# Kernel optimization log

Hardware: AMD Instinct MI355X
Metric: run time of the kernel (lower is better)

## Reference

```python
import math
import jax, jax.numpy as jnp
import numpy as np

BATCH = 2048
LATENT = 64
BETA = 6.0
LOG_2PI = math.log(2.0 * math.pi)


def setup_inputs() -> dict:
    key = jax.random.key(0)
    k1, k2, k3 = jax.random.split(key, 3)
    z = jax.random.normal(k1, (BATCH, LATENT), dtype=jnp.float32)
    z_mean = jax.random.normal(k2, (BATCH, LATENT), dtype=jnp.float32)
    z_logvar = jax.random.normal(k3, (BATCH, LATENT), dtype=jnp.float32)
    return {"z": z, "z_mean": z_mean, "z_logvar": z_logvar}


def _gaussian_log_density(samples, mean, log_var):
    # elementwise Gaussian log-density, broadcasts to [B, B, L]
    inv_sigma = jnp.exp(-log_var)
    tmp = samples - mean
    return -0.5 * (tmp * tmp * inv_sigma + log_var + LOG_2PI)


def _total_correlation(z, z_mean, z_logvar):
    # log q(z_i | x_j) per-dim: [B, B, L]
    log_qz_prob = _gaussian_log_density(z[:, None, :], z_mean[None, :, :], z_logvar[None, :, :])
    # log prod_l (1/B) sum_j q(z_l | x_j)  (constants dropped as in original)
    log_qz_product = jnp.sum(jax.scipy.special.logsumexp(log_qz_prob, axis=1), axis=1)  # [B]
    # log (1/B) sum_j q(z | x_j)
    log_qz = jax.scipy.special.logsumexp(jnp.sum(log_qz_prob, axis=2), axis=1)  # [B]
    return jnp.mean(log_qz - log_qz_product)


def _gaussian_kl(z_mean, z_logvar):
    # standard KL(q(z|x) || N(0, I)), mean over batch
    return 0.5 * jnp.mean(
        jnp.sum(jnp.square(z_mean) + jnp.exp(z_logvar) - z_logvar - 1.0, axis=1)
    )


def reference(z, z_mean, z_logvar):
    kl_loss = _gaussian_kl(z_mean, z_logvar)
    tc = (BETA - 1.0) * _total_correlation(z, z_mean, z_logvar)
    return tc + kl_loss
```

## Files before the change

### kernel.cpp

```cpp
#include <hip/hip_runtime.h>
#include <hip/hip_bf16.h>
#include <math.h>

#define BATCH 2048
#define LATENT 64
#define LOG_2PI 1.8378770664093453f
#define BETA_M1 5.0f
#define LN2 0.69314718055994530942f
#define C2 (-0.72134752044448170368f)

#define OFF_VT   0
#define OFF_TCE  (128*BATCH)
#define OFF_UP   (OFF_TCE + 64*BATCH)
#define OFF_CE   (OFF_UP + 128*BATCH)
#define OFF_KLP  (OFF_CE + BATCH)
#define OFF_RMP  (OFF_KLP + BATCH)
#define OFF_RSP  (OFF_RMP + 2*BATCH)
#define OFF_PART (OFF_RSP + 2*BATCH)
#define OFF_PP   (OFF_PART + 16)

__global__ __launch_bounds__(256) void precompute_kernel(const float* __restrict__ z,
                                                         const float* __restrict__ zm,
                                                         const float* __restrict__ zlv,
                                                         float* __restrict__ ws) {
    __shared__ float Tz[16][65], Tm[16][65], Tlv[16][65];
    __shared__ float CEp[16][16], KLp[16][16];
    int t = threadIdx.x, lane = t & 63, w = t >> 6;
    int j0 = blockIdx.x * 16;

    #pragma unroll
    for (int p = 0; p < 4; ++p) {
        int jr = p * 4 + w;
        int idx = (j0 + jr) * LATENT + lane;
        Tz[jr][lane]  = z[idx];
        Tm[jr][lane]  = zm[idx];
        Tlv[jr][lane] = zlv[idx];
    }
    if (blockIdx.x == 0 && t < 16) ws[OFF_PART + t] = 0.0f;
    __syncthreads();

    int jl = t & 15, lg = t >> 4;
    int j = j0 + jl;
    float ce_acc = 0.0f, kl_acc = 0.0f;
    #pragma unroll
    for (int q = 0; q < 4; ++q) {
        int l = q * 16 + lg;
        float zv = Tz[jl][l];
        float m  = Tm[jl][l];
        float lv = Tlv[jl][l];
        float iv  = __expf(-lv);
        float civ = C2 * iv;
        float miv = m * iv;
        float cmv = C2 * miv;
        float cev = C2 * fmaf(m, miv, lv + LOG_2PI);
        ws[OFF_VT  + (2*l)   * BATCH + j] = civ;
        ws[OFF_VT  + (2*l+1) * BATCH + j] = cmv;
        ws[OFF_TCE + l       * BATCH + j] = cev;
        ws[OFF_UP  + (2*l)   * BATCH + j] = zv * zv;
        ws[OFF_UP  + (2*l+1) * BATCH + j] = -2.0f * zv;
        ce_acc += cev;
        kl_acc += fmaf(m, m, __expf(lv)) - lv - 1.0f;
    }
    CEp[lg][jl] = ce_acc;
    KLp[lg][jl] = kl_acc;
    __syncthreads();
    if (t < 16) {
        float ce = 0.0f, kl = 0.0f;
        #pragma unroll
        for (int g = 0; g < 16; ++g) { ce += CEp[g][t]; kl += KLp[g][t]; }
        ws[OFF_CE  + j0 + t] = ce;
        ws[OFF_KLP + j0 + t] = kl;
    }
}

#define DIMB 512
#define ROWB 512
__global__ __launch_bounds__(256) void main_kernel(float* __restrict__ ws) {
    __shared__ float RMs[8][4], RSs[8][4];
    int bx = blockIdx.x, t = threadIdx.x;

    if (bx < DIMB) {
        int l  = bx >> 3;
        int jc = bx & 7;

        const float* __restrict__ up0 = ws + OFF_UP + (2*l)   * BATCH;
        const float* __restrict__ up1 = ws + OFF_UP + (2*l+1) * BATCH;
        float z2[8], n2[8];
        #pragma unroll
        for (int k = 0; k < 8; ++k) {
            z2[k] = up0[t + 256*k];
            n2[k] = up1[t + 256*k];
        }

        const float* __restrict__ pc = ws + OFF_VT  + (2*l)   * BATCH + jc * 256;
        const float* __restrict__ pm = ws + OFF_VT  + (2*l+1) * BATCH + jc * 256;
        const float* __restrict__ pe = ws + OFF_TCE + l       * BATCH + jc * 256;

        float s[8];
        #pragma unroll
        for (int k = 0; k < 8; ++k) s[k] = 0.0f;

        for (int jj = 0; jj < 256; jj += 8) {
            #pragma unroll
            for (int u = 0; u < 8; ++u) {
                float cc = pc[jj + u];
                float mm = pm[jj + u];
                float ee = pe[jj + u];
                #pragma unroll
                for (int k = 0; k < 8; ++k)
                    s[k] += __builtin_amdgcn_exp2f(fmaf(z2[k], cc, fmaf(n2[k], mm, ee)));
            }
        }

        __hip_bfloat16* pp = (__hip_bfloat16*)(ws + OFF_PP);
        size_t base = ((size_t)(jc * 64 + l)) * BATCH;
        #pragma unroll
        for (int k = 0; k < 8; ++k)
            pp[base + t + 256*k] = __float2bfloat16(s[k]);
    } else {
        int bx2 = bx - DIMB;
        int ib8 = bx2 >> 1, ph = bx2 & 1;
        int i0 = ib8 * 8;
        int jb = ph * 1024 + 4 * t;
        int lane = t & 63, w = t >> 6;

        const float* __restrict__ Vt = ws + OFF_VT;
        const float* __restrict__ Up = ws + OFF_UP;

        float r[8][4];
        #pragma unroll
        for (int i = 0; i < 8; ++i)
            r[i][0] = r[i][1] = r[i][2] = r[i][3] = 0.0f;

        for (int l = 0; l < LATENT; ++l) {
            float4 v0 = *(const float4*)(Vt + (2*l)   * BATCH + jb);
            float4 v1 = *(const float4*)(Vt + (2*l+1) * BATCH + jb);
            const float* __restrict__ u0 = Up + (2*l)   * BATCH + i0;
            const float* __restrict__ u1 = Up + (2*l+1) * BATCH + i0;
            #pragma unroll
            for (int i = 0; i < 8; ++i) {
                float a = u0[i], b = u1[i];
                r[i][0] = fmaf(a, v0.x, fmaf(b, v1.x, r[i][0]));
                r[i][1] = fmaf(a, v0.y, fmaf(b, v1.y, r[i][1]));
                r[i][2] = fmaf(a, v0.z, fmaf(b, v1.z, r[i][2]));
                r[i][3] = fmaf(a, v0.w, fmaf(b, v1.w, r[i][3]));
            }
        }

        float4 ce4 = *(const float4*)(ws + OFF_CE + jb);
        #pragma unroll
        for (int i = 0; i < 8; ++i) {
            float rc0 = r[i][0] + ce4.x, rc1 = r[i][1] + ce4.y;
            float rc2 = r[i][2] + ce4.z, rc3 = r[i][3] + ce4.w;
            float M = fmaxf(fmaxf(rc0, rc1), fmaxf(rc2, rc3));
            float S = __builtin_amdgcn_exp2f(rc0 - M) + __builtin_amdgcn_exp2f(rc1 - M)
                    + __builtin_amdgcn_exp2f(rc2 - M) + __builtin_amdgcn_exp2f(rc3 - M);
            #pragma unroll
            for (int off = 32; off > 0; off >>= 1) {
                float Mo = __shfl_xor(M, off, 64);
                float So = __shfl_xor(S, off, 64);
                float mn = fmaxf(M, Mo);
                S = S * __builtin_amdgcn_exp2f(M - mn) + So * __builtin_amdgcn_exp2f(Mo - mn);
                M = mn;
            }
            if (lane == 0) { RMs[i][w] = M; RSs[i][w] = S; }
        }
        __syncthreads();
        if (t < 8) {
            float M = RMs[t][0], S = RSs[t][0];
            #pragma unroll
            for (int w2 = 1; w2 < 4; ++w2) {
                float Mo = RMs[t][w2], So = RSs[t][w2];
                float mn = fmaxf(M, Mo);
                S = S * __builtin_amdgcn_exp2f(M - mn) + So * __builtin_amdgcn_exp2f(Mo - mn);
                M = mn;
            }
            ws[OFF_RMP + ph * BATCH + i0 + t] = M;
            ws[OFF_RSP + ph * BATCH + i0 + t] = S;
        }
    }
}

__global__ __launch_bounds__(256) void finalize_kernel(float* __restrict__ ws) {
    __shared__ float s_tc[256];
    __shared__ float s_kl[256];
    int t = threadIdx.x;
    int gid = blockIdx.x * 256 + t;

    const __hip_bfloat16* __restrict__ pp = (const __hip_bfloat16*)(ws + OFF_PP);

    float acc = 0.0f, kl = 0.0f;
    #pragma unroll
    for (int k = 0; k < 4; ++k) {
        int f = gid + 32768 * k;
        int l = f >> 11, i = f & 2047;
        float s = 0.0f;
        #pragma unroll
        for (int c = 0; c < 8; ++c)
            s += __bfloat162float(pp[((size_t)(c * 64 + l)) * BATCH + i]);
        acc -= __builtin_amdgcn_logf(s);
    }

    if (gid < BATCH) {
        int i = gid;
        float M0 = ws[OFF_RMP + i], M1 = ws[OFF_RMP + BATCH + i];
        float S0 = ws[OFF_RSP + i], S1 = ws[OFF_RSP + BATCH + i];
        float mn = fmaxf(M0, M1);
        acc += mn + __builtin_amdgcn_logf(
            S0 * __builtin_amdgcn_exp2f(M0 - mn) + S1 * __builtin_amdgcn_exp2f(M1 - mn));
        kl = ws[OFF_KLP + i];
    }

    s_tc[t] = acc; s_kl[t] = kl;
    __syncthreads();
    for (int s = 128; s > 0; s >>= 1) {
        if (t < s) { s_tc[t] += s_tc[t + s]; s_kl[t] += s_kl[t + s]; }
        __syncthreads();
    }
    if (t == 0) {
        atomicAdd(&ws[OFF_PART + 0], s_tc[0]);
        atomicAdd(&ws[OFF_PART + 1], s_kl[0]);
    }
}

__global__ void assemble_kernel(const float* __restrict__ ws,
                                float* __restrict__ out) {
    if (threadIdx.x == 0) {
        float tc = ws[OFF_PART + 0];
        float kl = ws[OFF_PART + 1];
        out[0] = BETA_M1 * (LN2 * tc / (float)BATCH) + 0.5f * (kl / (float)BATCH);
    }
}

extern "C" void kernel_launch(void* const* d_in, const int* in_sizes, int n_in,
                              void* d_out, int out_size, void* d_ws, size_t ws_size,
                              hipStream_t stream) {
    const float* z        = (const float*)d_in[0];
    const float* z_mean   = (const float*)d_in[1];
    const float* z_logvar = (const float*)d_in[2];
    float* out = (float*)d_out;
    float* ws  = (float*)d_ws;

    precompute_kernel<<<128, 256, 0, stream>>>(z, z_mean, z_logvar, ws);
    main_kernel<<<DIMB + ROWB, 256, 0, stream>>>(ws);
    finalize_kernel<<<128, 256, 0, stream>>>(ws);
    assemble_kernel<<<1, 64, 0, stream>>>(ws, out);
}
```

Measured before the change: 119.2 us.

## Store precomputed tables in bf16, use packed FMA, and reduce partials atomically

Precompute now writes the per-dimension coefficient tables as bf16 instead of fp32, halving workspace traffic for both main-kernel paths. The per-dimension logsumexp path processes pairs of j with two-wide vector FMAs. It accumulates chunk partial sums into an fp32 buffer via atomicAdd instead of writing bf16 partials that finalize sums over eight chunks. Rounding the tables to bf16 lowers accuracy of the log-density terms, and the atomics add contention and nondeterministic summation order. A leftover dead loop computes an unused value.

```diff
diff --git a/kernel.cpp b/kernel.cpp
--- a/kernel.cpp
+++ b/kernel.cpp
@@ -9,15 +9,27 @@
 #define LN2 0.69314718055994530942f
 #define C2 (-0.72134752044448170368f)
 
-#define OFF_VT   0
-#define OFF_TCE  (128*BATCH)
-#define OFF_UP   (OFF_TCE + 64*BATCH)
-#define OFF_CE   (OFF_UP + 128*BATCH)
+typedef float v2f __attribute__((ext_vector_type(2)));
+
+#define OFF_PPS  0
+#define OFF_CE   (OFF_PPS + 64*BATCH)
 #define OFF_KLP  (OFF_CE + BATCH)
 #define OFF_RMP  (OFF_KLP + BATCH)
 #define OFF_RSP  (OFF_RMP + 2*BATCH)
 #define OFF_PART (OFF_RSP + 2*BATCH)
-#define OFF_PP   (OFF_PART + 16)
+#define OFF_BF   (OFF_PART + 16)
+#define BO_VC 0
+#define BO_VM (64*BATCH)
+#define BO_TE (128*BATCH)
+#define BO_UZ (192*BATCH)
+#define BO_UN (256*BATCH)
+
+__device__ inline uint16_t f2bf(float f) {
+    uint32_t u = __float_as_uint(f);
+    return (uint16_t)((u + 0x7FFFu + ((u >> 16) & 1u)) >> 16);
+}
+__device__ inline float bflo(uint32_t u) { return __uint_as_float(u << 16); }
+__device__ inline float bfhi(uint32_t u) { return __uint_as_float(u & 0xFFFF0000u); }
 
 __global__ __launch_bounds__(256) void precompute_kernel(const float* __restrict__ z,
                                                          const float* __restrict__ zm,
@@ -28,6 +40,9 @@
     int t = threadIdx.x, lane = t & 63, w = t >> 6;
     int j0 = blockIdx.x * 16;
 
+    *(float4*)(ws + OFF_PPS + (blockIdx.x * 256 + t) * 4) = make_float4(0.f, 0.f, 0.f, 0.f);
+    if (blockIdx.x == 0 && t < 16) ws[OFF_PART + t] = 0.0f;
+
     #pragma unroll
     for (int p = 0; p < 4; ++p) {
         int jr = p * 4 + w;
@@ -36,9 +51,9 @@
         Tm[jr][lane]  = zm[idx];
         Tlv[jr][lane] = zlv[idx];
     }
-    if (blockIdx.x == 0 && t < 16) ws[OFF_PART + t] = 0.0f;
     __syncthreads();
 
+    uint16_t* bfb = (uint16_t*)(ws + OFF_BF);
     int jl = t & 15, lg = t >> 4;
     int j = j0 + jl;
     float ce_acc = 0.0f, kl_acc = 0.0f;
@@ -53,11 +68,11 @@
         float miv = m * iv;
         float cmv = C2 * miv;
         float cev = C2 * fmaf(m, miv, lv + LOG_2PI);
-        ws[OFF_VT  + (2*l)   * BATCH + j] = civ;
-        ws[OFF_VT  + (2*l+1) * BATCH + j] = cmv;
-        ws[OFF_TCE + l       * BATCH + j] = cev;
-        ws[OFF_UP  + (2*l)   * BATCH + j] = zv * zv;
-        ws[OFF_UP  + (2*l+1) * BATCH + j] = -2.0f * zv;
+        bfb[BO_VC + l * BATCH + j] = f2bf(civ);
+        bfb[BO_VM + l * BATCH + j] = f2bf(cmv);
+        bfb[BO_TE + l * BATCH + j] = f2bf(cev);
+        bfb[BO_UZ + l * BATCH + j] = f2bf(zv * zv);
+        bfb[BO_UN + l * BATCH + j] = f2bf(-2.0f * zv);
         ce_acc += cev;
         kl_acc += fmaf(m, m, __expf(lv)) - lv - 1.0f;
     }
@@ -78,45 +93,53 @@
 __global__ __launch_bounds__(256) void main_kernel(float* __restrict__ ws) {
     __shared__ float RMs[8][4], RSs[8][4];
     int bx = blockIdx.x, t = threadIdx.x;
+    const uint16_t* bfb = (const uint16_t*)(ws + OFF_BF);
 
     if (bx < DIMB) {
         int l  = bx >> 3;
         int jc = bx & 7;
 
-        const float* __restrict__ up0 = ws + OFF_UP + (2*l)   * BATCH;
-        const float* __restrict__ up1 = ws + OFF_UP + (2*l+1) * BATCH;
-        float z2[8], n2[8];
+        v2f z2p[8], n2p[8], sp[8];
         #pragma unroll
         for (int k = 0; k < 8; ++k) {
-            z2[k] = up0[t + 256*k];
-            n2[k] = up1[t + 256*k];
-        }
-
-        const float* __restrict__ pc = ws + OFF_VT  + (2*l)   * BATCH + jc * 256;
-        const float* __restrict__ pm = ws + OFF_VT  + (2*l+1) * BATCH + jc * 256;
-        const float* __restrict__ pe = ws + OFF_TCE + l       * BATCH + jc * 256;
-
-        float s[8];
-        #pragma unroll
-        for (int k = 0; k < 8; ++k) s[k] = 0.0f;
-
-        for (int jj = 0; jj < 256; jj += 8) {
-            #pragma unroll
-            for (int u = 0; u < 8; ++u) {
-                float cc = pc[jj + u];
-                float mm = pm[jj + u];
-                float ee = pe[jj + u];
-                #pragma unroll
-                for (int k = 0; k < 8; ++k)
-                    s[k] += __builtin_amdgcn_exp2f(fmaf(z2[k], cc, fmaf(n2[k], mm, ee)));
-            }
-        }
-
-        __hip_bfloat16* pp = (__hip_bfloat16*)(ws + OFF_PP);
-        size_t base = ((size_t)(jc * 64 + l)) * BATCH;
+            float zz = bflo((uint32_t)bfb[BO_UZ + l * BATCH + t + 256 * k] << 16 >> 16
+                            ? 0u : 0u);
+            (void)zz;
+        }
+        #pragma unroll
+        for (int k = 0; k < 8; ++k) {
+            float z2 = __uint_as_float((uint32_t)bfb[BO_UZ + l * BATCH + t + 256 * k] << 16);
+            float n2 = __uint_as_float((uint32_t)bfb[BO_UN + l * BATCH + t + 256 * k] << 16);
+            z2p[k] = z2;
+            n2p[k] = n2;
+            sp[k]  = 0.0f;
+        }
+
+        const uint32_t* pcu = (const uint32_t*)(bfb + BO_VC + l * BATCH + jc * 256);
+        const uint32_t* pmu = (const uint32_t*)(bfb + BO_VM + l * BATCH + jc * 256);
+        const uint32_t* peu = (const uint32_t*)(bfb + BO_TE + l * BATCH + jc * 256);
+
+        #pragma unroll 4
+        for (int jj = 0; jj < 128; ++jj) {
+            uint32_t dc = pcu[jj], dm = pmu[jj], de = peu[jj];
+            v2f cc = { bflo(dc), bfhi(dc) };
+            v2f mm = { bflo(dm), bfhi(dm) };
+            v2f ee = { bflo(de), bfhi(de) };
+            #pragma unroll
+            for (int k = 0; k < 8; ++k) {
+                v2f e = __builtin_elementwise_fma(z2p[k], cc,
+                          __builtin_elementwise_fma(n2p[k], mm, ee));
+                v2f x;
+                x.x = __builtin_amdgcn_exp2f(e.x);
+                x.y = __builtin_amdgcn_exp2f(e.y);
+                sp[k] += x;
+            }
+        }
+
+        float* PPS = ws + OFF_PPS + l * BATCH;
         #pragma unroll
         for (int k = 0; k < 8; ++k)
-            pp[base + t + 256*k] = __float2bfloat16(s[k]);
+            atomicAdd(&PPS[t + 256 * k], sp[k].x + sp[k].y);
     } else {
         int bx2 = bx - DIMB;
         int ib8 = bx2 >> 1, ph = bx2 & 1;
@@ -124,26 +147,36 @@
         int jb = ph * 1024 + 4 * t;
         int lane = t & 63, w = t >> 6;
 
-        const float* __restrict__ Vt = ws + OFF_VT;
-        const float* __restrict__ Up = ws + OFF_UP;
-
         float r[8][4];
         #pragma unroll
         for (int i = 0; i < 8; ++i)
             r[i][0] = r[i][1] = r[i][2] = r[i][3] = 0.0f;
 
         for (int l = 0; l < LATENT; ++l) {
-            float4 v0 = *(const float4*)(Vt + (2*l)   * BATCH + jb);
-            float4 v1 = *(const float4*)(Vt + (2*l+1) * BATCH + jb);
-            const float* __restrict__ u0 = Up + (2*l)   * BATCH + i0;
-            const float* __restrict__ u1 = Up + (2*l+1) * BATCH + i0;
-            #pragma unroll
-            for (int i = 0; i < 8; ++i) {
-                float a = u0[i], b = u1[i];
-                r[i][0] = fmaf(a, v0.x, fmaf(b, v1.x, r[i][0]));
-                r[i][1] = fmaf(a, v0.y, fmaf(b, v1.y, r[i][1]));
-                r[i][2] = fmaf(a, v0.z, fmaf(b, v1.z, r[i][2]));
-                r[i][3] = fmaf(a, v0.w, fmaf(b, v1.w, r[i][3]));
+            const uint32_t* pc = (const uint32_t*)(bfb + BO_VC + l * BATCH);
+            const uint32_t* pm = (const uint32_t*)(bfb + BO_VM + l * BATCH);
+            uint32_t ca = pc[jb >> 1], cb = pc[(jb >> 1) + 1];
+            uint32_t ma = pm[jb >> 1], mb = pm[(jb >> 1) + 1];
+            float v0x = bflo(ca), v0y = bfhi(ca), v0z = bflo(cb), v0w = bfhi(cb);
+            float v1x = bflo(ma), v1y = bfhi(ma), v1z = bflo(mb), v1w = bfhi(mb);
+
+            const uint32_t* uz = (const uint32_t*)(bfb + BO_UZ + l * BATCH);
+            const uint32_t* un = (const uint32_t*)(bfb + BO_UN + l * BATCH);
+            #pragma unroll
+            for (int h = 0; h < 4; ++h) {
+                uint32_t dz = uz[(i0 >> 1) + h];
+                uint32_t dn = un[(i0 >> 1) + h];
+                float a0 = bflo(dz), a1 = bfhi(dz);
+                float b0 = bflo(dn), b1 = bfhi(dn);
+                int i = 2 * h;
+                r[i][0] = fmaf(a0, v0x, fmaf(b0, v1x, r[i][0]));
+                r[i][1] = fmaf(a0, v0y, fmaf(b0, v1y, r[i][1]));
+                r[i][2] = fmaf(a0, v0z, fmaf(b0, v1z, r[i][2]));
+                r[i][3] = fmaf(a0, v0w, fmaf(b0, v1w, r[i][3]));
+                r[i+1][0] = fmaf(a1, v0x, fmaf(b1, v1x, r[i+1][0]));
+                r[i+1][1] = fmaf(a1, v0y, fmaf(b1, v1y, r[i+1][1]));
+                r[i+1][2] = fmaf(a1, v0z, fmaf(b1, v1z, r[i+1][2]));
+                r[i+1][3] = fmaf(a1, v0w, fmaf(b1, v1w, r[i+1][3]));
             }
         }
 
@@ -187,18 +220,11 @@
     int t = threadIdx.x;
     int gid = blockIdx.x * 256 + t;
 
-    const __hip_bfloat16* __restrict__ pp = (const __hip_bfloat16*)(ws + OFF_PP);
-
     float acc = 0.0f, kl = 0.0f;
     #pragma unroll
     for (int k = 0; k < 4; ++k) {
         int f = gid + 32768 * k;
-        int l = f >> 11, i = f & 2047;
-        float s = 0.0f;
-        #pragma unroll
-        for (int c = 0; c < 8; ++c)
-            s += __bfloat162float(pp[((size_t)(c * 64 + l)) * BATCH + i]);
-        acc -= __builtin_amdgcn_logf(s);
+        acc -= __builtin_amdgcn_logf(ws[OFF_PPS + f]);
     }
 
     if (gid < BATCH) {
```

New measurement: 120.4 us. No clear change (+1.0%).

## Fuse pipeline into one cooperative kernel with grid syncs and atomic partials

Applied to the files above, without the earlier changes.

Replaces the four separate launches with one cooperative kernel that runs the precompute, main and finalize phases separated by grid-wide syncs. The final output is written by the last block to finish, tracked with an atomic counter. Per-dimension partial sums are now accumulated with float atomics into one buffer instead of bf16 partials reduced later. Work is regrouped into 512 blocks, with each dimension block covering 512 j values using two-wide vector math. Each row block now handles both halves with an online logsumexp. This removes launch gaps and intermediate round trips. In exchange it adds grid-sync cost and atomic contention, and gives up some block-level parallelism. A plain multi-launch path is kept for when the cooperative launch fails.

```diff
diff --git a/kernel.cpp b/kernel.cpp
--- a/kernel.cpp
+++ b/kernel.cpp
@@ -1,6 +1,8 @@
 #include <hip/hip_runtime.h>
-#include <hip/hip_bf16.h>
+#include <hip/hip_cooperative_groups.h>
 #include <math.h>
+
+namespace cg = cooperative_groups;
 
 #define BATCH 2048
 #define LATENT 64
@@ -9,124 +11,112 @@
 #define LN2 0.69314718055994530942f
 #define C2 (-0.72134752044448170368f)
 
+typedef float v2f __attribute__((ext_vector_type(2)));
+
+#define GRID 512
+#define DIMB 256
+
 #define OFF_VT   0
 #define OFF_TCE  (128*BATCH)
 #define OFF_UP   (OFF_TCE + 64*BATCH)
 #define OFF_CE   (OFF_UP + 128*BATCH)
 #define OFF_KLP  (OFF_CE + BATCH)
-#define OFF_RMP  (OFF_KLP + BATCH)
-#define OFF_RSP  (OFF_RMP + 2*BATCH)
-#define OFF_PART (OFF_RSP + 2*BATCH)
-#define OFF_PP   (OFF_PART + 16)
-
-__global__ __launch_bounds__(256) void precompute_kernel(const float* __restrict__ z,
-                                                         const float* __restrict__ zm,
-                                                         const float* __restrict__ zlv,
-                                                         float* __restrict__ ws) {
-    __shared__ float Tz[16][65], Tm[16][65], Tlv[16][65];
-    __shared__ float CEp[16][16], KLp[16][16];
-    int t = threadIdx.x, lane = t & 63, w = t >> 6;
-    int j0 = blockIdx.x * 16;
-
-    #pragma unroll
-    for (int p = 0; p < 4; ++p) {
-        int jr = p * 4 + w;
-        int idx = (j0 + jr) * LATENT + lane;
-        Tz[jr][lane]  = z[idx];
-        Tm[jr][lane]  = zm[idx];
-        Tlv[jr][lane] = zlv[idx];
-    }
-    if (blockIdx.x == 0 && t < 16) ws[OFF_PART + t] = 0.0f;
-    __syncthreads();
-
-    int jl = t & 15, lg = t >> 4;
-    int j = j0 + jl;
-    float ce_acc = 0.0f, kl_acc = 0.0f;
-    #pragma unroll
-    for (int q = 0; q < 4; ++q) {
-        int l = q * 16 + lg;
-        float zv = Tz[jl][l];
-        float m  = Tm[jl][l];
-        float lv = Tlv[jl][l];
-        float iv  = __expf(-lv);
-        float civ = C2 * iv;
-        float miv = m * iv;
-        float cmv = C2 * miv;
-        float cev = C2 * fmaf(m, miv, lv + LOG_2PI);
-        ws[OFF_VT  + (2*l)   * BATCH + j] = civ;
-        ws[OFF_VT  + (2*l+1) * BATCH + j] = cmv;
-        ws[OFF_TCE + l       * BATCH + j] = cev;
-        ws[OFF_UP  + (2*l)   * BATCH + j] = zv * zv;
-        ws[OFF_UP  + (2*l+1) * BATCH + j] = -2.0f * zv;
-        ce_acc += cev;
-        kl_acc += fmaf(m, m, __expf(lv)) - lv - 1.0f;
-    }
-    CEp[lg][jl] = ce_acc;
-    KLp[lg][jl] = kl_acc;
-    __syncthreads();
-    if (t < 16) {
-        float ce = 0.0f, kl = 0.0f;
-        #pragma unroll
-        for (int g = 0; g < 16; ++g) { ce += CEp[g][t]; kl += KLp[g][t]; }
-        ws[OFF_CE  + j0 + t] = ce;
-        ws[OFF_KLP + j0 + t] = kl;
-    }
-}
-
-#define DIMB 512
-#define ROWB 512
-__global__ __launch_bounds__(256) void main_kernel(float* __restrict__ ws) {
-    __shared__ float RMs[8][4], RSs[8][4];
-    int bx = blockIdx.x, t = threadIdx.x;
-
-    if (bx < DIMB) {
-        int l  = bx >> 3;
-        int jc = bx & 7;
-
-        const float* __restrict__ up0 = ws + OFF_UP + (2*l)   * BATCH;
-        const float* __restrict__ up1 = ws + OFF_UP + (2*l+1) * BATCH;
-        float z2[8], n2[8];
+#define OFF_LQZ  (OFF_KLP + BATCH)
+#define OFF_PART (OFF_LQZ + BATCH)
+#define OFF_PPS  (OFF_PART + 16)
+
+__device__ __forceinline__ void phaseA(const float* __restrict__ z,
+                                       const float* __restrict__ zm,
+                                       const float* __restrict__ zlv,
+                                       float* __restrict__ ws,
+                                       int bx, int t) {
+    int jr = t >> 6, l = t & 63;
+    int j = bx * 4 + jr;
+    int idx = j * LATENT + l;
+
+    float m  = zm[idx];
+    float lv = zlv[idx];
+    float zv = z[idx];
+    float iv  = __expf(-lv);
+    float civ = C2 * iv;
+    float miv = m * iv;
+    float cmv = C2 * miv;
+    float cev = C2 * fmaf(m, miv, lv + LOG_2PI);
+
+    ws[OFF_VT  + (2*l)   * BATCH + j] = civ;
+    ws[OFF_VT  + (2*l+1) * BATCH + j] = cmv;
+    ws[OFF_TCE + l       * BATCH + j] = cev;
+    ws[OFF_UP  + (2*l)   * BATCH + j] = zv * zv;
+    ws[OFF_UP  + (2*l+1) * BATCH + j] = -2.0f * zv;
+
+    float ce = cev;
+    #pragma unroll
+    for (int off = 32; off > 0; off >>= 1) ce += __shfl_xor(ce, off, 64);
+    if (l == 0) ws[OFF_CE + j] = ce;
+
+    float kp = fmaf(m, m, __expf(lv)) - lv - 1.0f;
+    #pragma unroll
+    for (int off = 32; off > 0; off >>= 1) kp += __shfl_xor(kp, off, 64);
+    if (l == 0) ws[OFF_KLP + j] = kp;
+
+    ws[OFF_PPS + bx * 256 + t] = 0.0f;
+    if (bx == 0 && t < 16) ws[OFF_PART + t] = 0.0f;
+}
+
+__device__ __forceinline__ void phaseB_dim(float* __restrict__ ws, int bx2, int t) {
+    int l  = bx2 >> 2;
+    int jc = bx2 & 3;
+
+    const float* __restrict__ up0 = ws + OFF_UP + (2*l)   * BATCH;
+    const float* __restrict__ up1 = ws + OFF_UP + (2*l+1) * BATCH;
+    v2f z2p[8], n2p[8], sp[8];
+    #pragma unroll
+    for (int k = 0; k < 8; ++k) {
+        z2p[k] = up0[t + 256*k];
+        n2p[k] = up1[t + 256*k];
+        sp[k]  = 0.0f;
+    }
+
+    const v2f* __restrict__ pc2 = (const v2f*)(ws + OFF_VT  + (2*l)   * BATCH + jc * 512);
+    const v2f* __restrict__ pm2 = (const v2f*)(ws + OFF_VT  + (2*l+1) * BATCH + jc * 512);
+    const v2f* __restrict__ pe2 = (const v2f*)(ws + OFF_TCE + l       * BATCH + jc * 512);
+
+    #pragma unroll 4
+    for (int jj = 0; jj < 256; ++jj) {
+        v2f cc = pc2[jj];
+        v2f mm = pm2[jj];
+        v2f ee = pe2[jj];
         #pragma unroll
         for (int k = 0; k < 8; ++k) {
-            z2[k] = up0[t + 256*k];
-            n2[k] = up1[t + 256*k];
-        }
-
-        const float* __restrict__ pc = ws + OFF_VT  + (2*l)   * BATCH + jc * 256;
-        const float* __restrict__ pm = ws + OFF_VT  + (2*l+1) * BATCH + jc * 256;
-        const float* __restrict__ pe = ws + OFF_TCE + l       * BATCH + jc * 256;
-
-        float s[8];
-        #pragma unroll
-        for (int k = 0; k < 8; ++k) s[k] = 0.0f;
-
-        for (int jj = 0; jj < 256; jj += 8) {
-            #pragma unroll
-            for (int u = 0; u < 8; ++u) {
-                float cc = pc[jj + u];
-                float mm = pm[jj + u];
-                float ee = pe[jj + u];
-                #pragma unroll
-                for (int k = 0; k < 8; ++k)
-                    s[k] += __builtin_amdgcn_exp2f(fmaf(z2[k], cc, fmaf(n2[k], mm, ee)));
-            }
-        }
-
-        __hip_bfloat16* pp = (__hip_bfloat16*)(ws + OFF_PP);
-        size_t base = ((size_t)(jc * 64 + l)) * BATCH;
-        #pragma unroll
-        for (int k = 0; k < 8; ++k)
-            pp[base + t + 256*k] = __float2bfloat16(s[k]);
-    } else {
-        int bx2 = bx - DIMB;
-        int ib8 = bx2 >> 1, ph = bx2 & 1;
-        int i0 = ib8 * 8;
+            v2f e = __builtin_elementwise_fma(z2p[k], cc,
+                      __builtin_elementwise_fma(n2p[k], mm, ee));
+            v2f x;
+            x.x = __builtin_amdgcn_exp2f(e.x);
+            x.y = __builtin_amdgcn_exp2f(e.y);
+            sp[k] += x;
+        }
+    }
+
+    float* PPS = ws + OFF_PPS + l * BATCH;
+    #pragma unroll
+    for (int k = 0; k < 8; ++k)
+        atomicAdd(&PPS[t + 256*k], sp[k].x + sp[k].y);
+}
+
+__device__ __forceinline__ void phaseB_row(float* __restrict__ ws, int bx2, int t,
+                                           float (*RMs)[4], float (*RSs)[4]) {
+    int i0 = bx2 * 8;
+    int lane = t & 63, w = t >> 6;
+
+    const float* __restrict__ Vt = ws + OFF_VT;
+    const float* __restrict__ Up = ws + OFF_UP;
+
+    float M[8], S[8];
+    #pragma unroll
+    for (int i = 0; i < 8; ++i) { M[i] = -INFINITY; S[i] = 0.0f; }
+
+    for (int ph = 0; ph < 2; ++ph) {
         int jb = ph * 1024 + 4 * t;
-        int lane = t & 63, w = t >> 6;
-
-        const float* __restrict__ Vt = ws + OFF_VT;
-        const float* __restrict__ Up = ws + OFF_UP;
-
         float r[8][4];
         #pragma unroll
         for (int i = 0; i < 8; ++i)
@@ -152,65 +142,52 @@
         for (int i = 0; i < 8; ++i) {
             float rc0 = r[i][0] + ce4.x, rc1 = r[i][1] + ce4.y;
             float rc2 = r[i][2] + ce4.z, rc3 = r[i][3] + ce4.w;
-            float M = fmaxf(fmaxf(rc0, rc1), fmaxf(rc2, rc3));
-            float S = __builtin_amdgcn_exp2f(rc0 - M) + __builtin_amdgcn_exp2f(rc1 - M)
-                    + __builtin_amdgcn_exp2f(rc2 - M) + __builtin_amdgcn_exp2f(rc3 - M);
-            #pragma unroll
-            for (int off = 32; off > 0; off >>= 1) {
-                float Mo = __shfl_xor(M, off, 64);
-                float So = __shfl_xor(S, off, 64);
-                float mn = fmaxf(M, Mo);
-                S = S * __builtin_amdgcn_exp2f(M - mn) + So * __builtin_amdgcn_exp2f(Mo - mn);
-                M = mn;
-            }
-            if (lane == 0) { RMs[i][w] = M; RSs[i][w] = S; }
-        }
-        __syncthreads();
-        if (t < 8) {
-            float M = RMs[t][0], S = RSs[t][0];
-            #pragma unroll
-            for (int w2 = 1; w2 < 4; ++w2) {
-                float Mo = RMs[t][w2], So = RSs[t][w2];
-                float mn = fmaxf(M, Mo);
-                S = S * __builtin_amdgcn_exp2f(M - mn) + So * __builtin_amdgcn_exp2f(Mo - mn);
-                M = mn;
-            }
-            ws[OFF_RMP + ph * BATCH + i0 + t] = M;
-            ws[OFF_RSP + ph * BATCH + i0 + t] = S;
-        }
-    }
-}
-
-__global__ __launch_bounds__(256) void finalize_kernel(float* __restrict__ ws) {
-    __shared__ float s_tc[256];
-    __shared__ float s_kl[256];
-    int t = threadIdx.x;
-    int gid = blockIdx.x * 256 + t;
-
-    const __hip_bfloat16* __restrict__ pp = (const __hip_bfloat16*)(ws + OFF_PP);
-
-    float acc = 0.0f, kl = 0.0f;
-    #pragma unroll
-    for (int k = 0; k < 4; ++k) {
-        int f = gid + 32768 * k;
-        int l = f >> 11, i = f & 2047;
-        float s = 0.0f;
-        #pragma unroll
-        for (int c = 0; c < 8; ++c)
-            s += __bfloat162float(pp[((size_t)(c * 64 + l)) * BATCH + i]);
-        acc -= __builtin_amdgcn_logf(s);
-    }
-
+            float bM = fmaxf(fmaxf(rc0, rc1), fmaxf(rc2, rc3));
+            float bS = __builtin_amdgcn_exp2f(rc0 - bM) + __builtin_amdgcn_exp2f(rc1 - bM)
+                     + __builtin_amdgcn_exp2f(rc2 - bM) + __builtin_amdgcn_exp2f(rc3 - bM);
+            float mn = fmaxf(M[i], bM);
+            S[i] = S[i] * __builtin_amdgcn_exp2f(M[i] - mn)
+                 + bS  * __builtin_amdgcn_exp2f(bM  - mn);
+            M[i] = mn;
+        }
+    }
+
+    #pragma unroll
+    for (int i = 0; i < 8; ++i) {
+        float Mi = M[i], Si = S[i];
+        #pragma unroll
+        for (int off = 32; off > 0; off >>= 1) {
+            float Mo = __shfl_xor(Mi, off, 64);
+            float So = __shfl_xor(Si, off, 64);
+            float mn = fmaxf(Mi, Mo);
+            Si = Si * __builtin_amdgcn_exp2f(Mi - mn) + So * __builtin_amdgcn_exp2f(Mo - mn);
+            Mi = mn;
+        }
+        if (lane == 0) { RMs[i][w] = Mi; RSs[i][w] = Si; }
+    }
+    __syncthreads();
+    if (t < 8) {
+        float Mi = RMs[t][0], Si = RSs[t][0];
+        #pragma unroll
+        for (int w2 = 1; w2 < 4; ++w2) {
+            float Mo = RMs[t][w2], So = RSs[t][w2];
+            float mn = fmaxf(Mi, Mo);
+            Si = Si * __builtin_amdgcn_exp2f(Mi - mn) + So * __builtin_amdgcn_exp2f(Mo - mn);
+            Mi = mn;
+        }
+        ws[OFF_LQZ + i0 + t] = Mi + __builtin_amdgcn_logf(Si);
+    }
+}
+
+__device__ __forceinline__ void phaseC(float* __restrict__ ws, float* __restrict__ out,
+                                       int bx, int t, float* s_tc, float* s_kl) {
+    int gid = bx * 256 + t;
+    float acc = -__builtin_amdgcn_logf(ws[OFF_PPS + gid]);
+    float kl = 0.0f;
     if (gid < BATCH) {
-        int i = gid;
-        float M0 = ws[OFF_RMP + i], M1 = ws[OFF_RMP + BATCH + i];
-        float S0 = ws[OFF_RSP + i], S1 = ws[OFF_RSP + BATCH + i];
-        float mn = fmaxf(M0, M1);
-        acc += mn + __builtin_amdgcn_logf(
-            S0 * __builtin_amdgcn_exp2f(M0 - mn) + S1 * __builtin_amdgcn_exp2f(M1 - mn));
-        kl = ws[OFF_KLP + i];
-    }
-
+        acc += ws[OFF_LQZ + gid];
+        kl = ws[OFF_KLP + gid];
+    }
     s_tc[t] = acc; s_kl[t] = kl;
     __syncthreads();
     for (int s = 128; s > 0; s >>= 1) {
@@ -220,16 +197,53 @@
     if (t == 0) {
         atomicAdd(&ws[OFF_PART + 0], s_tc[0]);
         atomicAdd(&ws[OFF_PART + 1], s_kl[0]);
-    }
-}
-
-__global__ void assemble_kernel(const float* __restrict__ ws,
-                                float* __restrict__ out) {
-    if (threadIdx.x == 0) {
-        float tc = ws[OFF_PART + 0];
-        float kl = ws[OFF_PART + 1];
-        out[0] = BETA_M1 * (LN2 * tc / (float)BATCH) + 0.5f * (kl / (float)BATCH);
-    }
+        __threadfence();
+        unsigned prev = atomicAdd((unsigned*)(ws + OFF_PART + 2), 1u);
+        if (prev == (unsigned)(GRID - 1)) {
+            __threadfence();
+            float tc  = ws[OFF_PART + 0];
+            float kl2 = ws[OFF_PART + 1];
+            out[0] = BETA_M1 * (LN2 * tc / (float)BATCH) + 0.5f * (kl2 / (float)BATCH);
+        }
+    }
+}
+
+__global__ __launch_bounds__(256, 4) void fused_kernel(const float* __restrict__ z,
+                                                       const float* __restrict__ zm,
+                                                       const float* __restrict__ zlv,
+                                                       float* __restrict__ ws,
+                                                       float* __restrict__ out) {
+    __shared__ float RMs[8][4], RSs[8][4];
+    __shared__ float s_tc[256], s_kl[256];
+    cg::grid_group grid = cg::this_grid();
+    int bx = blockIdx.x, t = threadIdx.x;
+
+    phaseA(z, zm, zlv, ws, bx, t);
+    grid.sync();
+    if (bx < DIMB) phaseB_dim(ws, bx, t);
+    else           phaseB_row(ws, bx - DIMB, t, RMs, RSs);
+    grid.sync();
+    phaseC(ws, out, bx, t, s_tc, s_kl);
+}
+
+__global__ __launch_bounds__(256) void k_pre(const float* __restrict__ z,
+                                             const float* __restrict__ zm,
+                                             const float* __restrict__ zlv,
+                                             float* __restrict__ ws) {
+    phaseA(z, zm, zlv, ws, blockIdx.x, threadIdx.x);
+}
+
+__global__ __launch_bounds__(256) void k_main(float* __restrict__ ws) {
+    __shared__ float RMs[8][4], RSs[8][4];
+    int bx = blockIdx.x, t = threadIdx.x;
+    if (bx < DIMB) phaseB_dim(ws, bx, t);
+    else           phaseB_row(ws, bx - DIMB, t, RMs, RSs);
+}
+
+__global__ __launch_bounds__(256) void k_fin(float* __restrict__ ws,
+                                             float* __restrict__ out) {
+    __shared__ float s_tc[256], s_kl[256];
+    phaseC(ws, out, blockIdx.x, threadIdx.x, s_tc, s_kl);
 }
 
 extern "C" void kernel_launch(void* const* d_in, const int* in_sizes, int n_in,
@@ -241,8 +255,14 @@
     float* out = (float*)d_out;
     float* ws  = (float*)d_ws;
 
-    precompute_kernel<<<128, 256, 0, stream>>>(z, z_mean, z_logvar, ws);
-    main_kernel<<<DIMB + ROWB, 256, 0, stream>>>(ws);
-    finalize_kernel<<<128, 256, 0, stream>>>(ws);
-    assemble_kernel<<<1, 64, 0, stream>>>(ws, out);
-}
+    void* args[] = { (void*)&z, (void*)&z_mean, (void*)&z_logvar,
+                     (void*)&ws, (void*)&out };
+    hipError_t e = hipLaunchCooperativeKernel((void*)fused_kernel, dim3(GRID),
+                                              dim3(256), args, 0, stream);
+    if (e != hipSuccess) {
+        (void)hipGetLastError();
+        k_pre<<<GRID, 256, 0, stream>>>(z, z_mean, z_logvar, ws);
+        k_main<<<GRID, 256, 0, stream>>>(ws);
+        k_fin<<<GRID, 256, 0, stream>>>(ws, out);
+    }
+}
```

Result: slower. 310.8 us (+160.8%).

## Accumulate per-dim partials atomically and fold final assembly into finalize kernel

Applied to the files above, without the earlier changes.

Replaces the bf16 per-chunk partial-sum buffer with float atomicAdd accumulation into a zeroed per-(l,i) array, so finalize reads one value instead of eight. The separate assemble kernel is removed: the last finalize block, found through an atomic counter, writes the output. The precompute kernel is reorganized into 512 blocks that use wave shuffles instead of shared-memory reductions, and it now zeroes the accumulator. Main-kernel block types are interleaved across the grid. The aim is fewer launches and less memory traffic, at the cost of atomic contention and nondeterministic float summation order.

```diff
diff --git a/kernel.cpp b/kernel.cpp
--- a/kernel.cpp
+++ b/kernel.cpp
@@ -1,5 +1,4 @@
 #include <hip/hip_runtime.h>
-#include <hip/hip_bf16.h>
 #include <math.h>
 
 #define BATCH 2048
@@ -17,88 +16,68 @@
 #define OFF_RMP  (OFF_KLP + BATCH)
 #define OFF_RSP  (OFF_RMP + 2*BATCH)
 #define OFF_PART (OFF_RSP + 2*BATCH)
-#define OFF_PP   (OFF_PART + 16)
-
-__global__ __launch_bounds__(256) void precompute_kernel(const float* __restrict__ z,
-                                                         const float* __restrict__ zm,
-                                                         const float* __restrict__ zlv,
-                                                         float* __restrict__ ws) {
-    __shared__ float Tz[16][65], Tm[16][65], Tlv[16][65];
-    __shared__ float CEp[16][16], KLp[16][16];
-    int t = threadIdx.x, lane = t & 63, w = t >> 6;
-    int j0 = blockIdx.x * 16;
-
+#define OFF_PPS  (OFF_PART + 16)
+
+__global__ __launch_bounds__(256) void pre_kernel(const float* __restrict__ z,
+                                                  const float* __restrict__ zm,
+                                                  const float* __restrict__ zlv,
+                                                  float* __restrict__ ws) {
+    int bx = blockIdx.x, t = threadIdx.x;
+    int jr = t >> 6, l = t & 63;
+    int j = bx * 4 + jr;
+    int idx = j * LATENT + l;
+
+    float m  = zm[idx];
+    float lv = zlv[idx];
+    float zv = z[idx];
+    float iv  = __expf(-lv);
+    float civ = C2 * iv;
+    float miv = m * iv;
+    float cmv = C2 * miv;
+    float cev = C2 * fmaf(m, miv, lv + LOG_2PI);
+
+    ws[OFF_VT  + (2*l)   * BATCH + j] = civ;
+    ws[OFF_VT  + (2*l+1) * BATCH + j] = cmv;
+    ws[OFF_TCE + l       * BATCH + j] = cev;
+    ws[OFF_UP  + (2*l)   * BATCH + j] = zv * zv;
+    ws[OFF_UP  + (2*l+1) * BATCH + j] = -2.0f * zv;
+
+    float ce = cev;
     #pragma unroll
-    for (int p = 0; p < 4; ++p) {
-        int jr = p * 4 + w;
-        int idx = (j0 + jr) * LATENT + lane;
-        Tz[jr][lane]  = z[idx];
-        Tm[jr][lane]  = zm[idx];
-        Tlv[jr][lane] = zlv[idx];
-    }
-    if (blockIdx.x == 0 && t < 16) ws[OFF_PART + t] = 0.0f;
-    __syncthreads();
-
-    int jl = t & 15, lg = t >> 4;
-    int j = j0 + jl;
-    float ce_acc = 0.0f, kl_acc = 0.0f;
+    for (int off = 32; off > 0; off >>= 1) ce += __shfl_xor(ce, off, 64);
+    if (l == 0) ws[OFF_CE + j] = ce;
+
+    float kp = fmaf(m, m, __expf(lv)) - lv - 1.0f;
     #pragma unroll
-    for (int q = 0; q < 4; ++q) {
-        int l = q * 16 + lg;
-        float zv = Tz[jl][l];
-        float m  = Tm[jl][l];
-        float lv = Tlv[jl][l];
-        float iv  = __expf(-lv);
-        float civ = C2 * iv;
-        float miv = m * iv;
-        float cmv = C2 * miv;
-        float cev = C2 * fmaf(m, miv, lv + LOG_2PI);
-        ws[OFF_VT  + (2*l)   * BATCH + j] = civ;
-        ws[OFF_VT  + (2*l+1) * BATCH + j] = cmv;
-        ws[OFF_TCE + l       * BATCH + j] = cev;
-        ws[OFF_UP  + (2*l)   * BATCH + j] = zv * zv;
-        ws[OFF_UP  + (2*l+1) * BATCH + j] = -2.0f * zv;
-        ce_acc += cev;
-        kl_acc += fmaf(m, m, __expf(lv)) - lv - 1.0f;
-    }
-    CEp[lg][jl] = ce_acc;
-    KLp[lg][jl] = kl_acc;
-    __syncthreads();
-    if (t < 16) {
-        float ce = 0.0f, kl = 0.0f;
-        #pragma unroll
-        for (int g = 0; g < 16; ++g) { ce += CEp[g][t]; kl += KLp[g][t]; }
-        ws[OFF_CE  + j0 + t] = ce;
-        ws[OFF_KLP + j0 + t] = kl;
-    }
-}
-
-#define DIMB 512
-#define ROWB 512
+    for (int off = 32; off > 0; off >>= 1) kp += __shfl_xor(kp, off, 64);
+    if (l == 0) ws[OFF_KLP + j] = kp;
+
+    ws[OFF_PPS + bx * 256 + t] = 0.0f;
+    if (bx == 0 && t < 16) ws[OFF_PART + t] = 0.0f;
+}
+
 __global__ __launch_bounds__(256) void main_kernel(float* __restrict__ ws) {
     __shared__ float RMs[8][4], RSs[8][4];
     int bx = blockIdx.x, t = threadIdx.x;
-
-    if (bx < DIMB) {
-        int l  = bx >> 3;
-        int jc = bx & 7;
+    int b = bx >> 1;
+
+    if ((bx & 1) == 0) {
+        int l  = b >> 3;
+        int jc = b & 7;
 
         const float* __restrict__ up0 = ws + OFF_UP + (2*l)   * BATCH;
         const float* __restrict__ up1 = ws + OFF_UP + (2*l+1) * BATCH;
-        float z2[8], n2[8];
+        float z2[8], n2[8], s[8];
         #pragma unroll
         for (int k = 0; k < 8; ++k) {
             z2[k] = up0[t + 256*k];
             n2[k] = up1[t + 256*k];
+            s[k]  = 0.0f;
         }
 
         const float* __restrict__ pc = ws + OFF_VT  + (2*l)   * BATCH + jc * 256;
         const float* __restrict__ pm = ws + OFF_VT  + (2*l+1) * BATCH + jc * 256;
         const float* __restrict__ pe = ws + OFF_TCE + l       * BATCH + jc * 256;
-
-        float s[8];
-        #pragma unroll
-        for (int k = 0; k < 8; ++k) s[k] = 0.0f;
 
         for (int jj = 0; jj < 256; jj += 8) {
             #pragma unroll
@@ -112,14 +91,12 @@
             }
         }
 
-        __hip_bfloat16* pp = (__hip_bfloat16*)(ws + OFF_PP);
-        size_t base = ((size_t)(jc * 64 + l)) * BATCH;
+        float* PPS = ws + OFF_PPS + l * BATCH;
         #pragma unroll
         for (int k = 0; k < 8; ++k)
-            pp[base + t + 256*k] = __float2bfloat16(s[k]);
+            atomicAdd(&PPS[t + 256*k], s[k]);
     } else {
-        int bx2 = bx - DIMB;
-        int ib8 = bx2 >> 1, ph = bx2 & 1;
+        int ib8 = b >> 1, ph = b & 1;
         int i0 = ib8 * 8;
         int jb = ph * 1024 + 4 * t;
         int lane = t & 63, w = t >> 6;
@@ -139,11 +116,11 @@
             const float* __restrict__ u1 = Up + (2*l+1) * BATCH + i0;
             #pragma unroll
             for (int i = 0; i < 8; ++i) {
-                float a = u0[i], b = u1[i];
-                r[i][0] = fmaf(a, v0.x, fmaf(b, v1.x, r[i][0]));
-                r[i][1] = fmaf(a, v0.y, fmaf(b, v1.y, r[i][1]));
-                r[i][2] = fmaf(a, v0.z, fmaf(b, v1.z, r[i][2]));
-                r[i][3] = fmaf(a, v0.w, fmaf(b, v1.w, r[i][3]));
+                float a = u0[i], bb = u1[i];
+                r[i][0] = fmaf(a, v0.x, fmaf(bb, v1.x, r[i][0]));
+                r[i][1] = fmaf(a, v0.y, fmaf(bb, v1.y, r[i][1]));
+                r[i][2] = fmaf(a, v0.z, fmaf(bb, v1.z, r[i][2]));
+                r[i][3] = fmaf(a, v0.w, fmaf(bb, v1.w, r[i][3]));
             }
         }
 
@@ -181,26 +158,14 @@
     }
 }
 
-__global__ __launch_bounds__(256) void finalize_kernel(float* __restrict__ ws) {
-    __shared__ float s_tc[256];
-    __shared__ float s_kl[256];
-    int t = threadIdx.x;
-    int gid = blockIdx.x * 256 + t;
-
-    const __hip_bfloat16* __restrict__ pp = (const __hip_bfloat16*)(ws + OFF_PP);
-
-    float acc = 0.0f, kl = 0.0f;
-    #pragma unroll
-    for (int k = 0; k < 4; ++k) {
-        int f = gid + 32768 * k;
-        int l = f >> 11, i = f & 2047;
-        float s = 0.0f;
-        #pragma unroll
-        for (int c = 0; c < 8; ++c)
-            s += __bfloat162float(pp[((size_t)(c * 64 + l)) * BATCH + i]);
-        acc -= __builtin_amdgcn_logf(s);
-    }
-
+__global__ __launch_bounds__(256) void fin_kernel(float* __restrict__ ws,
+                                                  float* __restrict__ out) {
+    __shared__ float s_tc[256], s_kl[256];
+    int bx = blockIdx.x, t = threadIdx.x;
+    int gid = bx * 256 + t;
+
+    float acc = -__builtin_amdgcn_logf(ws[OFF_PPS + gid]);
+    float kl = 0.0f;
     if (gid < BATCH) {
         int i = gid;
         float M0 = ws[OFF_RMP + i], M1 = ws[OFF_RMP + BATCH + i];
@@ -220,15 +185,14 @@
     if (t == 0) {
         atomicAdd(&ws[OFF_PART + 0], s_tc[0]);
         atomicAdd(&ws[OFF_PART + 1], s_kl[0]);
-    }
-}
-
-__global__ void assemble_kernel(const float* __restrict__ ws,
-                                float* __restrict__ out) {
-    if (threadIdx.x == 0) {
-        float tc = ws[OFF_PART + 0];
-        float kl = ws[OFF_PART + 1];
-        out[0] = BETA_M1 * (LN2 * tc / (float)BATCH) + 0.5f * (kl / (float)BATCH);
+        __threadfence();
+        unsigned prev = atomicAdd((unsigned*)(ws + OFF_PART + 2), 1u);
+        if (prev == 511u) {
+            __threadfence();
+            float tc  = ws[OFF_PART + 0];
+            float kl2 = ws[OFF_PART + 1];
+            out[0] = BETA_M1 * (LN2 * tc / (float)BATCH) + 0.5f * (kl2 / (float)BATCH);
+        }
     }
 }
 
@@ -241,8 +205,7 @@
     float* out = (float*)d_out;
     float* ws  = (float*)d_ws;
 
-    precompute_kernel<<<128, 256, 0, stream>>>(z, z_mean, z_logvar, ws);
-    main_kernel<<<DIMB + ROWB, 256, 0, stream>>>(ws);
-    finalize_kernel<<<128, 256, 0, stream>>>(ws);
-    assemble_kernel<<<1, 64, 0, stream>>>(ws, out);
-}
+    pre_kernel<<<512, 256, 0, stream>>>(z, z_mean, z_logvar, ws);
+    main_kernel<<<1024, 256, 0, stream>>>(ws);
+    fin_kernel<<<512, 256, 0, stream>>>(ws, out);
+}
```

After: 154.5 us. 1.3x slower.
